# Optimization experiments

Hardware: AMD Instinct MI355X
Metric: run time of the kernel (lower is better)

Reference implementation:

```python
import jax, jax.numpy as jnp
import numpy as np

B, N, H, V = 2048, 16, 512, 780  # trees, nodes per tree, hidden size, vocab size


def _topology():
    """Build one random tree, replicate across B trees, and precompute the
    BFS level schedule on the non-backtracking line graph (as DGL's
    level_order: reversed(edges_back) = up edges leaves-first, then
    edges = down edges root-first)."""
    rng = np.random.default_rng(0)
    parent = np.zeros(N, dtype=np.int64)
    for i in range(1, N):
        parent[i] = rng.integers(0, i)
    depth = np.zeros(N, dtype=np.int64)
    for i in range(1, N):
        depth[i] = depth[parent[i]] + 1
    Epc = 2 * (N - 1)  # directed edges per tree
    src = np.zeros(Epc, dtype=np.int64)
    dst = np.zeros(Epc, dtype=np.int64)
    for i in range(1, N):
        src[2 * (i - 1)] = parent[i]; dst[2 * (i - 1)] = i          # down edge
        src[2 * (i - 1) + 1] = i;     dst[2 * (i - 1) + 1] = parent[i]  # up edge
    # line-graph predecessors of edge e=(u->v): edges f=(w->u) with w != v
    preds = [[f for f in range(Epc) if dst[f] == src[e] and src[f] != dst[e]]
             for e in range(Epc)]
    P = max(1, max(len(p) for p in preds))
    preds_pad = np.full((Epc, P), -1, dtype=np.int64)
    for e, p in enumerate(preds):
        preds_pad[e, :len(p)] = p
    D = int(depth.max())
    levels = []
    for d in range(D, 0, -1):   # upward pass, deepest level first
        levels.append([2 * (i - 1) + 1 for i in range(1, N) if depth[i] == d])
    for d in range(1, D + 1):   # downward pass, root first
        levels.append([2 * (i - 1) for i in range(1, N) if depth[i] == d])
    E = B * Epc                 # index E is the zero dummy row
    offs = np.arange(B, dtype=np.int64) * Epc
    preds_full = np.where(preds_pad[None] >= 0,
                          preds_pad[None] + offs[:, None, None], E)
    preds_full = preds_full.reshape(E, P)
    preds_full = np.concatenate(
        [preds_full, np.full((1, P), E, dtype=np.int64)], axis=0)  # [E+1, P]
    Mmax = max(len(lv) for lv in levels) * B
    lv_arr = np.full((len(levels), Mmax), E, dtype=np.int64)
    for l, lv in enumerate(levels):
        ids = (np.asarray(lv, np.int64)[None] + offs[:, None]).reshape(-1)
        lv_arr[l, :ids.size] = ids
    edge_src = (src[None] + np.arange(B, dtype=np.int64)[:, None] * N).reshape(-1)
    root_children = [2 * (i - 1) + 1 for i in range(1, N) if parent[i] == 0]
    root_in = np.asarray(root_children, np.int64)[None] + offs[:, None]  # [B, R]
    root_nodes = np.arange(B, dtype=np.int64) * N
    return edge_src, preds_full, lv_arr, root_in, root_nodes


def setup_inputs() -> dict:
    key = jax.random.key(0)
    ks = jax.random.split(key, 11)
    edge_src, preds, levels, root_in, root_nodes = _topology()
    s1 = 1.0 / np.sqrt(H)
    s2 = 1.0 / np.sqrt(2 * H)
    return {
        "wid": jax.random.randint(ks[0], (B * N,), 0, V),
        "edge_src": jnp.asarray(edge_src),
        "preds": jnp.asarray(preds),
        "levels": jnp.asarray(levels),
        "root_in": jnp.asarray(root_in),
        "root_nodes": jnp.asarray(root_nodes),
        "emb": jax.random.normal(ks[1], (V, H), jnp.float32),
        "w_r": jax.random.normal(ks[2], (H, H), jnp.float32) * s1,
        "ur_w": jax.random.normal(ks[3], (H, H), jnp.float32) * s1,
        "ur_b": jax.random.normal(ks[4], (H,), jnp.float32) * s1,
        "wz_w": jax.random.normal(ks[5], (2 * H, H), jnp.float32) * s2,
        "wz_b": jax.random.normal(ks[6], (H,), jnp.float32) * s2,
        "wh_w": jax.random.normal(ks[7], (2 * H, H), jnp.float32) * s2,
        "wh_b": jax.random.normal(ks[8], (H,), jnp.float32) * s2,
        "wo_w": jax.random.normal(ks[9], (2 * H, H), jnp.float32) * s2,
        "wo_b": jax.random.normal(ks[10], (H,), jnp.float32) * s2,
    }


def reference(wid, edge_src, preds, levels, root_in, root_nodes,
              emb, w_r, ur_w, ur_b, wz_w, wz_b, wh_w, wh_b, wo_w, wo_b):
    E = edge_src.shape[0]
    Hd = emb.shape[1]
    x = emb[wid]                                           # [B*N, H]
    zero = jnp.zeros((1, Hd), x.dtype)
    sx_all = x[edge_src]                                   # src_x per edge
    src_x = jnp.concatenate([sx_all, zero], axis=0)        # [E+1, H], row E = 0
    src_x_r = jnp.concatenate([sx_all @ w_r, zero], axis=0)  # W_r (no bias)
    h = jnp.zeros((E + 1, Hd), x.dtype)
    for l in range(levels.shape[0]):                       # static BFS levels
        idx = levels[l]                                    # [M], padded with E
        p = preds[idx]                                     # [M, P]
        h_nei = h[p]                                       # [M, P, H]
        sum_h = h_nei.sum(axis=1)
        # GRUMessage: r = sigmoid(dst.src_x_r + U_r(src.h)); m = r * src.h
        r = jax.nn.sigmoid(src_x_r[idx][:, None, :] + h_nei @ ur_w + ur_b)
        sum_g = (r * h_nei).sum(axis=1)
        sx = src_x[idx]
        # GRUUpdate
        z = jax.nn.sigmoid(jnp.concatenate([sx, sum_h], axis=-1) @ wz_w + wz_b)
        pre_h = jnp.tanh(jnp.concatenate([sx, sum_g], axis=-1) @ wh_w + wh_b)
        h = h.at[idx].set((1.0 - z) * sum_h + z * pre_h)
        h = h.at[E].set(0.0)                               # keep dummy row zero
    h_edges = h[:E]                                        # edata['h']
    h_root = h[root_in].sum(axis=1)                        # pull into roots
    x_root = x[root_nodes]
    root_vec = jax.nn.relu(
        jnp.concatenate([x_root, h_root], axis=-1) @ wo_w + wo_b)
    return h_edges, root_vec
```

## Files before the change

### kernel.cpp

```cpp
#include <hip/hip_runtime.h>
#include <hip/hip_bf16.h>
#include <cstddef>

#define HD 512

typedef short s8v __attribute__((ext_vector_type(8)));
typedef short s4v __attribute__((ext_vector_type(4)));
typedef float fx4 __attribute__((ext_vector_type(4)));

#define MFMA(a, b, c) __builtin_amdgcn_mfma_f32_16x16x32_bf16((a), (b), (c), 0, 0, 0)

__device__ __forceinline__ unsigned short f2bf(float f) {
  unsigned int u = __float_as_uint(f);
  unsigned int r = (u + 0x7fffu + ((u >> 16) & 1u)) >> 16;
  return (unsigned short)r;
}
__device__ __forceinline__ float bf2f(unsigned short u) {
  return __uint_as_float(((unsigned int)u) << 16);
}

__device__ __forceinline__ size_t swz_off(int k, int n, int KT) {
  int kt = k >> 5, kr = k & 31;
  int nt = n >> 4, nr = n & 15;
  int lane = ((kr >> 3) << 4) | nr;
  int i = kr & 7;
  return ((((size_t)nt * KT + kt) * 64 + lane) << 3) + i;
}

__global__ void pack_kernel(const float* w_r, const float* ur, const float* wz, const float* wh,
                            const float* wo,
                            unsigned short* WR, unsigned short* WUR, unsigned short* WZf,
                            unsigned short* WHf, unsigned short* WO) {
  int idx = blockIdx.x * blockDim.x + threadIdx.x;
  int stride = gridDim.x * blockDim.x;
  for (int t = idx; t < 512 * 512; t += stride) {
    int k = t >> 9, n = t & 511;
    size_t o = swz_off(k, n, 16);
    WR[o] = f2bf(w_r[t]);
    WUR[o] = f2bf(ur[t]);
  }
  for (int t = idx; t < 1024 * 512; t += stride) {
    int k = t >> 9, n = t & 511;
    size_t o = swz_off(k, n, 32);
    WZf[o] = f2bf(wz[t]);
    WHf[o] = f2bf(wh[t]);
    WO[o] = f2bf(wo[t]);
  }
}

__global__ void embed_kernel(const int* wid, const float* emb, unsigned short* x_bf, int BN) {
  int idx = blockIdx.x * blockDim.x + threadIdx.x;
  int stride = gridDim.x * blockDim.x;
  int total = BN * (HD / 8);
  for (int t = idx; t < total; t += stride) {
    int nrow = t >> 6;
    int c8 = (t & 63) << 3;
    int w = wid[nrow];
    const float4* s = (const float4*)(emb + (size_t)w * HD + c8);
    float4 v0 = s[0], v1 = s[1];
    s8v o;
    o[0] = (short)f2bf(v0.x); o[1] = (short)f2bf(v0.y);
    o[2] = (short)f2bf(v0.z); o[3] = (short)f2bf(v0.w);
    o[4] = (short)f2bf(v1.x); o[5] = (short)f2bf(v1.y);
    o[6] = (short)f2bf(v1.z); o[7] = (short)f2bf(v1.w);
    *(s8v*)&x_bf[(size_t)nrow * HD + c8] = o;
  }
}

__global__ void schedule_kernel(const int* preds, int E, int Epc, int P, int* sched) {
  __shared__ int rnd[64];
  int t = threadIdx.x;
  rnd[t] = -1;
  __syncthreads();
  for (int it = 0; it <= Epc; ++it) {
    int newv = -1;
    if (t < Epc && rnd[t] < 0) {
      int mx = 0;
      bool ready = true;
      for (int q = 0; q < P; ++q) {
        int pe = preds[t * P + q];
        if (pe < E) {
          int rp = rnd[pe];
          if (rp < 0) ready = false;
          else if (rp + 1 > mx) mx = rp + 1;
        }
      }
      if (ready) newv = mx;
    }
    __syncthreads();
    if (newv >= 0) rnd[t] = newv;
    __syncthreads();
  }
  if (t == 0) {
    int R = 0;
    for (int e = 0; e < Epc; ++e) if (rnd[e] + 1 > R) R = rnd[e] + 1;
    if (R > 31) R = 31;
    sched[0] = R;
    for (int r = 0; r < 31; ++r) {
      int c = 0;
      if (r < R) {
        for (int e = 0; e < Epc; ++e) if (rnd[e] == r) { sched[33 + r * 32 + c] = e; ++c; }
      }
      sched[1 + r] = c;
    }
  }
}

__global__ __launch_bounds__(256) void gemm_xr_kernel(const unsigned short* x_bf,
                                                      const unsigned short* WR,
                                                      unsigned short* XR, int BN) {
  __shared__ unsigned short lA[32 * 40];
  int bt = blockIdx.x;
  int mt = bt >> 1, nt = bt & 1;
  int tid = threadIdx.x, lane = tid & 63, w = tid >> 6;
  int wm = w & 1, wn = w >> 1;
  int m0 = mt << 5;
  fx4 acc[8];
#pragma unroll
  for (int n = 0; n < 8; n++) { acc[n][0]=0.f; acc[n][1]=0.f; acc[n][2]=0.f; acc[n][3]=0.f; }
  int srow = tid >> 3, squad = tid & 7;
  int arow = (wm << 4) | (lane & 15), k8 = (lane >> 4) << 3;
  for (int kt = 0; kt < 16; ++kt) {
    const unsigned short* gp = x_bf + (size_t)(m0 + srow) * HD + (kt << 5) + (squad << 2);
    *(s4v*)&lA[srow * 40 + (squad << 2)] = *(const s4v*)gp;
    __syncthreads();
    s8v a = *(const s8v*)&lA[arow * 40 + k8];
#pragma unroll
    for (int n = 0; n < 8; n++) {
      int ntile = (nt << 4) + (wn << 3) + n;
      const s8v* bp = (const s8v*)(WR + ((((size_t)ntile << 4) + kt) * 64 + lane) * 8);
      acc[n] = MFMA(a, *bp, acc[n]);
    }
    __syncthreads();
  }
#pragma unroll
  for (int n = 0; n < 8; n++) {
    int gcol = (nt << 8) + (wn << 7) + (n << 4) + (lane & 15);
#pragma unroll
    for (int q = 0; q < 4; q++) {
      int row = (wm << 4) + ((lane >> 4) << 2) + q;
      XR[(size_t)(m0 + row) * 512 + gcol] = f2bf(acc[n][q]);
    }
  }
}

struct AP {
  const int* sched;
  const int* preds;
  const int* edge_src;
  const float* ur_b;
  const unsigned short* XR;
  const unsigned short* u_bf_c;
  unsigned short* A2h;
  unsigned short* A2g;
  int* eIdx;
  int* srcIdx;
  float* h;
  int B, Epc, P, E;
};

__global__ __launch_bounds__(256) void gatherA_kernel(AP p, int r) {
  const int cnt = p.sched[1 + r];
  if (cnt == 0) return;
  const int M = cnt * p.B;
  const int* lst = p.sched + 33 + r * 32;
  const int lane = threadIdx.x & 63;
  const int waveId = blockIdx.x * 4 + (threadIdx.x >> 6);
  const int totalWaves = gridDim.x * 4;
  for (int m = waveId; m < M; m += totalWaves) {
    const int j = m / p.B;
    const int b = m - j * p.B;
    const int e = b * p.Epc + lst[j];
    const int src = p.edge_src[e];
    if (lane == 0) { p.eIdx[m] = e; p.srcIdx[m] = src; }
    const int c0 = lane << 3;
    const s8v xr8 = *(const s8v*)&p.XR[(size_t)src * 512 + c0];
    float xb[8], ub[8], sh[8], sg[8];
#pragma unroll
    for (int i = 0; i < 8; i++) {
      xb[i] = bf2f((unsigned short)xr8[i]);
      ub[i] = p.ur_b[c0 + i];
      sh[i] = 0.f; sg[i] = 0.f;
    }
    for (int t = 0; t < p.P; ++t) {
      const int pe = p.preds[(size_t)e * p.P + t];
      if (pe >= p.E) continue;
      const float4* hp = (const float4*)(p.h + (size_t)pe * 512 + c0);
      const float4 h0 = hp[0], h1 = hp[1];
      const s8v u8 = *(const s8v*)&p.u_bf_c[(size_t)pe * 512 + c0];
      const float hv[8] = {h0.x, h0.y, h0.z, h0.w, h1.x, h1.y, h1.z, h1.w};
#pragma unroll
      for (int i = 0; i < 8; i++) {
        const float rr = 1.f / (1.f + __expf(-(xb[i] + bf2f((unsigned short)u8[i]) + ub[i])));
        sh[i] += hv[i];
        sg[i] += rr * hv[i];
      }
    }
    *(float4*)(p.h + (size_t)e * 512 + c0) = make_float4(sh[0], sh[1], sh[2], sh[3]);
    *(float4*)(p.h + (size_t)e * 512 + c0 + 4) = make_float4(sh[4], sh[5], sh[6], sh[7]);
    s8v shb, sgb;
#pragma unroll
    for (int i = 0; i < 8; i++) { shb[i] = (short)f2bf(sh[i]); sgb[i] = (short)f2bf(sg[i]); }
    *(s8v*)&p.A2h[(size_t)m * 512 + c0] = shb;
    *(s8v*)&p.A2g[(size_t)m * 512 + c0] = sgb;
  }
}

struct BP {
  const int* sched;
  const float* wz_b;
  const float* wh_b;
  const unsigned short* x_bf;
  const unsigned short* A2h;
  const unsigned short* A2g;
  const unsigned short* WZf;
  const unsigned short* WHf;
  const int* eIdx;
  const int* srcIdx;
  unsigned short* h_bf;
  float* h;
  int B;
};

__global__ __launch_bounds__(256) void gemmB_kernel(BP p, int r) {
  const int cnt = p.sched[1 + r];
  if (cnt == 0) return;
  const int M = cnt * p.B;
  const int nTiles = (M >> 6) << 2;
  __shared__ unsigned short lZ[2][64 * 40];
  __shared__ unsigned short lH[2][64 * 40];
  __shared__ int eL[64];
  __shared__ int sL[64];
  const int tid = threadIdx.x, lane = tid & 63, w = tid >> 6;
  const int wm = w & 1, wn = w >> 1;
  const int srow = tid >> 2, sc8 = (tid & 3) << 3;
  const int k8 = (lane >> 4) << 3;

  for (int t = blockIdx.x; t < nTiles; t += gridDim.x) {
    const int mt = t >> 2, nb = t & 3;
    const int m0 = mt << 6, n0 = nb << 7;
    if (tid < 64) { eL[tid] = p.eIdx[m0 + tid]; sL[tid] = p.srcIdx[m0 + tid]; }
    __syncthreads();
    fx4 aZ[8], aH[8];
#pragma unroll
    for (int i = 0; i < 8; i++) {
      aZ[i][0]=0.f; aZ[i][1]=0.f; aZ[i][2]=0.f; aZ[i][3]=0.f;
      aH[i][0]=0.f; aH[i][1]=0.f; aH[i][2]=0.f; aH[i][3]=0.f;
    }
    {
      const unsigned short* g = p.x_bf + (size_t)sL[srow] * 512 + sc8;
      *(s8v*)&lZ[0][srow * 40 + sc8] = *(const s8v*)g;
    }
    for (int kt = 0; kt < 32; ++kt) {
      const int cur = kt & 1;
      __syncthreads();
      if (kt < 31) {
        const int k2 = kt + 1;
        if (k2 < 16) {
          const unsigned short* g = p.x_bf + (size_t)sL[srow] * 512 + (k2 << 5) + sc8;
          *(s8v*)&lZ[cur ^ 1][srow * 40 + sc8] = *(const s8v*)g;
        } else {
          const size_t ro = (size_t)(m0 + srow) * 512 + ((k2 - 16) << 5) + sc8;
          *(s8v*)&lZ[cur ^ 1][srow * 40 + sc8] = *(const s8v*)&p.A2h[ro];
          *(s8v*)&lH[cur ^ 1][srow * 40 + sc8] = *(const s8v*)&p.A2g[ro];
        }
      }
      s8v az[2], ah[2];
#pragma unroll
      for (int mi = 0; mi < 2; ++mi) {
        const int ao = ((wm << 5) + (mi << 4) + (lane & 15)) * 40 + k8;
        az[mi] = *(const s8v*)&lZ[cur][ao];
        ah[mi] = (kt < 16) ? az[mi] : *(const s8v*)&lH[cur][ao];
      }
#pragma unroll
      for (int ni = 0; ni < 4; ++ni) {
        const int ntile = (n0 >> 4) + (wn << 2) + ni;
        const size_t boff = (((size_t)ntile * 32 + kt) * 64 + lane) << 3;
        const s8v bz = *(const s8v*)(p.WZf + boff);
        const s8v bh = *(const s8v*)(p.WHf + boff);
#pragma unroll
        for (int mi = 0; mi < 2; ++mi) {
          aZ[mi * 4 + ni] = MFMA(az[mi], bz, aZ[mi * 4 + ni]);
          aH[mi * 4 + ni] = MFMA(ah[mi], bh, aH[mi * 4 + ni]);
        }
      }
    }
#pragma unroll
    for (int mi = 0; mi < 2; ++mi) {
#pragma unroll
      for (int q = 0; q < 4; ++q) {
        const int row = (wm << 5) + (mi << 4) + ((lane >> 4) << 2) + q;
        const int e = eL[row];
#pragma unroll
        for (int ni = 0; ni < 4; ++ni) {
          const int col = n0 + (wn << 6) + (ni << 4) + (lane & 15);
          const size_t off = (size_t)e * 512 + col;
          float zpre = aZ[mi * 4 + ni][q] + p.wz_b[col];
          float hpre = aH[mi * 4 + ni][q] + p.wh_b[col];
          float zz = 1.f / (1.f + __expf(-zpre));
          float e2 = __expf(2.f * hpre);
          float th = 1.f - 2.f / (e2 + 1.f);
          float hn = (1.f - zz) * p.h[off] + zz * th;
          p.h[off] = hn;
          p.h_bf[off] = f2bf(hn);
        }
      }
    }
    __syncthreads();
  }
}

struct CP {
  const int* sched;
  const unsigned short* h_bf;
  const unsigned short* WUR;
  const int* eIdx;
  unsigned short* u_bf;
  int B;
};

__global__ __launch_bounds__(256) void gemmC_kernel(CP p, int r) {
  const int cnt = p.sched[1 + r];
  if (cnt == 0) return;
  const int M = cnt * p.B;
  const int nTiles = (M >> 6) << 2;
  __shared__ unsigned short lA[2][64 * 40];
  __shared__ int eL[64];
  const int tid = threadIdx.x, lane = tid & 63, w = tid >> 6;
  const int wm = w & 1, wn = w >> 1;
  const int srow = tid >> 2, sc8 = (tid & 3) << 3;
  const int k8 = (lane >> 4) << 3;

  for (int t = blockIdx.x; t < nTiles; t += gridDim.x) {
    const int mt = t >> 2, nb = t & 3;
    const int m0 = mt << 6, n0 = nb << 7;
    if (tid < 64) eL[tid] = p.eIdx[m0 + tid];
    __syncthreads();
    fx4 ac[8];
#pragma unroll
    for (int i = 0; i < 8; i++) { ac[i][0]=0.f; ac[i][1]=0.f; ac[i][2]=0.f; ac[i][3]=0.f; }
    {
      const unsigned short* g = p.h_bf + (size_t)eL[srow] * 512 + sc8;
      *(s8v*)&lA[0][srow * 40 + sc8] = *(const s8v*)g;
    }
    for (int kt = 0; kt < 16; ++kt) {
      const int cur = kt & 1;
      __syncthreads();
      if (kt < 15) {
        const unsigned short* g = p.h_bf + (size_t)eL[srow] * 512 + ((kt + 1) << 5) + sc8;
        *(s8v*)&lA[cur ^ 1][srow * 40 + sc8] = *(const s8v*)g;
      }
      s8v az[2];
#pragma unroll
      for (int mi = 0; mi < 2; ++mi) {
        az[mi] = *(const s8v*)&lA[cur][((wm << 5) + (mi << 4) + (lane & 15)) * 40 + k8];
      }
#pragma unroll
      for (int ni = 0; ni < 4; ++ni) {
        const int ntile = (n0 >> 4) + (wn << 2) + ni;
        const size_t boff = (((size_t)ntile << 4) + kt) * 64 + lane;
        const s8v bu = *(const s8v*)(p.WUR + (boff << 3));
#pragma unroll
        for (int mi = 0; mi < 2; ++mi) {
          ac[mi * 4 + ni] = MFMA(az[mi], bu, ac[mi * 4 + ni]);
        }
      }
    }
#pragma unroll
    for (int mi = 0; mi < 2; ++mi) {
#pragma unroll
      for (int q = 0; q < 4; ++q) {
        const int row = (wm << 5) + (mi << 4) + ((lane >> 4) << 2) + q;
        const int e = eL[row];
#pragma unroll
        for (int ni = 0; ni < 4; ++ni) {
          const int col = n0 + (wn << 6) + (ni << 4) + (lane & 15);
          p.u_bf[(size_t)e * 512 + col] = f2bf(ac[mi * 4 + ni][q]);
        }
      }
    }
    __syncthreads();
  }
}

__global__ void root_gather_kernel(const int* root_nodes, const int* root_in,
                                   const unsigned short* x_bf, const float* h,
                                   unsigned short* Aroot, int B, int R0) {
  int lane = threadIdx.x & 63;
  int waveId = blockIdx.x * (blockDim.x >> 6) + (threadIdx.x >> 6);
  int totalWaves = gridDim.x * (blockDim.x >> 6);
  for (int b = waveId; b < B; b += totalWaves) {
    int c0 = lane << 3;
    int nd = root_nodes[b];
    *(s8v*)&Aroot[(size_t)b * 1024 + c0] = *(const s8v*)&x_bf[(size_t)nd * HD + c0];
    float s[8];
#pragma unroll
    for (int i = 0; i < 8; i++) s[i] = 0.f;
    for (int t = 0; t < R0; ++t) {
      int e = root_in[b * R0 + t];
      const float4* hp = (const float4*)(h + (size_t)e * HD + c0);
      float4 h0 = hp[0], h1 = hp[1];
      s[0] += h0.x; s[1] += h0.y; s[2] += h0.z; s[3] += h0.w;
      s[4] += h1.x; s[5] += h1.y; s[6] += h1.z; s[7] += h1.w;
    }
    s8v sb;
#pragma unroll
    for (int i = 0; i < 8; i++) sb[i] = (short)f2bf(s[i]);
    *(s8v*)&Aroot[(size_t)b * 1024 + 512 + c0] = sb;
  }
}

__global__ __launch_bounds__(256) void gemm_root_kernel(const unsigned short* Aroot,
                                                        const unsigned short* WO,
                                                        const float* wo_b, float* out, int B) {
  __shared__ unsigned short lA[32 * 40];
  int tid = threadIdx.x, lane = tid & 63, w = tid >> 6;
  int wm = w & 1, wn = w >> 1;
  int bt = blockIdx.x;
  int mt = bt >> 1, nt = bt & 1;
  int m0 = mt << 5;
  fx4 ac[8];
#pragma unroll
  for (int n = 0; n < 8; n++) { ac[n][0]=0.f; ac[n][1]=0.f; ac[n][2]=0.f; ac[n][3]=0.f; }
  int srow = tid >> 3, squad = tid & 7;
  int arow = (wm << 4) | (lane & 15), k8 = (lane >> 4) << 3;
  for (int kt = 0; kt < 32; ++kt) {
    const unsigned short* g = Aroot + (size_t)(m0 + srow) * 1024 + (kt << 5) + (squad << 2);
    *(s4v*)&lA[srow * 40 + (squad << 2)] = *(const s4v*)g;
    __syncthreads();
    s8v a = *(const s8v*)&lA[arow * 40 + k8];
#pragma unroll
    for (int n = 0; n < 8; n++) {
      int ntile = (nt << 4) + (wn << 3) + n;
      size_t boff = ((((size_t)ntile * 32) + kt) * 64 + lane) << 3;
      ac[n] = MFMA(a, *(const s8v*)(WO + boff), ac[n]);
    }
    __syncthreads();
  }
#pragma unroll
  for (int q = 0; q < 4; q++) {
    int row = (wm << 4) + ((lane >> 4) << 2) + q;
    int m = m0 + row;
#pragma unroll
    for (int n = 0; n < 8; n++) {
      int col = (nt << 8) + (wn << 7) + (n << 4) + (lane & 15);
      float v = ac[n][q] + wo_b[col];
      out[(size_t)m * HD + col] = v > 0.f ? v : 0.f;
    }
  }
}

extern "C" void kernel_launch(void* const* d_in, const int* in_sizes, int n_in,
                              void* d_out, int out_size, void* d_ws, size_t ws_size,
                              hipStream_t stream) {
  const int* wid = (const int*)d_in[0];
  const int* edge_src = (const int*)d_in[1];
  const int* preds = (const int*)d_in[2];
  const int* root_in = (const int*)d_in[4];
  const int* root_nodes = (const int*)d_in[5];
  const float* emb = (const float*)d_in[6];
  const float* w_r = (const float*)d_in[7];
  const float* ur_w = (const float*)d_in[8];
  const float* ur_b = (const float*)d_in[9];
  const float* wz_w = (const float*)d_in[10];
  const float* wz_b = (const float*)d_in[11];
  const float* wh_w = (const float*)d_in[12];
  const float* wh_b = (const float*)d_in[13];
  const float* wo_w = (const float*)d_in[14];
  const float* wo_b = (const float*)d_in[15];

  const int BN = in_sizes[0];
  const int E = in_sizes[1];
  const int Bt = in_sizes[5];
  const int Epc = E / Bt;
  const int P = in_sizes[2] / (E + 1);
  const int R0 = in_sizes[4] / Bt;

  float* h = (float*)d_out;

  char* wp = (char*)d_ws;
  auto alloc = [&](size_t bytes) {
    char* r = wp;
    wp += (bytes + 255) & ~(size_t)255;
    return r;
  };
  unsigned short* x_bf = (unsigned short*)alloc((size_t)BN * 512 * 2);
  unsigned short* XR = (unsigned short*)alloc((size_t)BN * 512 * 2);
  unsigned short* h_bf = (unsigned short*)alloc((size_t)E * 512 * 2);
  unsigned short* u_bf = (unsigned short*)alloc((size_t)E * 512 * 2);
  unsigned short* A2h = (unsigned short*)alloc((size_t)E * 512 * 2);
  unsigned short* A2g = (unsigned short*)alloc((size_t)E * 512 * 2);
  int* eIdx = (int*)alloc((size_t)E * 4);
  int* srcIdx = (int*)alloc((size_t)E * 4);
  unsigned short* WR = (unsigned short*)alloc((size_t)512 * 512 * 2);
  unsigned short* WUR = (unsigned short*)alloc((size_t)512 * 512 * 2);
  unsigned short* WZf = (unsigned short*)alloc((size_t)1024 * 512 * 2);
  unsigned short* WHf = (unsigned short*)alloc((size_t)1024 * 512 * 2);
  unsigned short* WO = (unsigned short*)alloc((size_t)1024 * 512 * 2);
  unsigned short* Aroot = (unsigned short*)alloc((size_t)Bt * 1024 * 2);
  int* sched = (int*)alloc(8192);

  hipLaunchKernelGGL(pack_kernel, dim3(512), dim3(256), 0, stream,
                     w_r, ur_w, wz_w, wh_w, wo_w, WR, WUR, WZf, WHf, WO);
  hipLaunchKernelGGL(embed_kernel, dim3(1024), dim3(256), 0, stream, wid, emb, x_bf, BN);
  hipLaunchKernelGGL(schedule_kernel, dim3(1), dim3(64), 0, stream, preds, E, Epc, P, sched);
  hipLaunchKernelGGL(gemm_xr_kernel, dim3((BN / 32) * 2), dim3(256), 0, stream, x_bf, WR, XR, BN);

  AP ap;
  ap.sched = sched; ap.preds = preds; ap.edge_src = edge_src;
  ap.ur_b = ur_b; ap.XR = XR; ap.u_bf_c = u_bf;
  ap.A2h = A2h; ap.A2g = A2g; ap.eIdx = eIdx; ap.srcIdx = srcIdx;
  ap.h = h; ap.B = Bt; ap.Epc = Epc; ap.P = P; ap.E = E;

  BP bp;
  bp.sched = sched; bp.wz_b = wz_b; bp.wh_b = wh_b;
  bp.x_bf = x_bf; bp.A2h = A2h; bp.A2g = A2g;
  bp.WZf = WZf; bp.WHf = WHf;
  bp.eIdx = eIdx; bp.srcIdx = srcIdx;
  bp.h_bf = h_bf; bp.h = h; bp.B = Bt;

  CP cp;
  cp.sched = sched; cp.h_bf = h_bf; cp.WUR = WUR;
  cp.eIdx = eIdx; cp.u_bf = u_bf; cp.B = Bt;

  for (int r = 0; r < Epc && r < 31; ++r) {
    hipLaunchKernelGGL(gatherA_kernel, dim3(1024), dim3(256), 0, stream, ap, r);
    hipLaunchKernelGGL(gemmB_kernel, dim3(2048), dim3(256), 0, stream, bp, r);
    hipLaunchKernelGGL(gemmC_kernel, dim3(2048), dim3(256), 0, stream, cp, r);
  }

  hipLaunchKernelGGL(root_gather_kernel, dim3(512), dim3(256), 0, stream,
                     root_nodes, root_in, x_bf, h, Aroot, Bt, R0);
  hipLaunchKernelGGL(gemm_root_kernel, dim3((Bt / 32) * 2), dim3(256), 0, stream,
                     Aroot, WO, wo_b, h + (size_t)E * 512, Bt);
}
```

Baseline: 1.127 ms.

## Precompute x-side Z/H projections once per node and halve per-level GEMM K

The x-half of the z and h gate GEMMs is hoisted out of the per-level loop into one upfront GEMM that produces the r, z and h x-projections together, using a concatenated weight matrix. Per-level gemmB now only multiplies the 512-wide neighbour sums and adds the precomputed x terms in the epilogue. gemmB writes a compact row-ordered bf16 copy of h, so gemmC reads contiguously instead of gathering by edge index. The change also widens the LDS K-step to 64, swizzles tile order across blocks, and halves the grid sizes. In exchange it adds an XP buffer three times the width of the old XR and extra scattered bf16 reads in the gemmB epilogue.

```diff
diff --git a/kernel.cpp b/kernel.cpp
--- a/kernel.cpp
+++ b/kernel.cpp
@@ -29,22 +29,28 @@
 
 __global__ void pack_kernel(const float* w_r, const float* ur, const float* wz, const float* wh,
                             const float* wo,
-                            unsigned short* WR, unsigned short* WUR, unsigned short* WZf,
-                            unsigned short* WHf, unsigned short* WO) {
+                            unsigned short* W1, unsigned short* WZB, unsigned short* WHB,
+                            unsigned short* WUR, unsigned short* WO) {
   int idx = blockIdx.x * blockDim.x + threadIdx.x;
   int stride = gridDim.x * blockDim.x;
+  for (int t = idx; t < 512 * 1536; t += stride) {
+    int k = t / 1536, n = t - k * 1536;
+    float v;
+    if (n < 512) v = w_r[k * 512 + n];
+    else if (n < 1024) v = wz[k * 512 + (n - 512)];
+    else v = wh[k * 512 + (n - 1024)];
+    W1[swz_off(k, n, 16)] = f2bf(v);
+  }
   for (int t = idx; t < 512 * 512; t += stride) {
     int k = t >> 9, n = t & 511;
     size_t o = swz_off(k, n, 16);
-    WR[o] = f2bf(w_r[t]);
-    WUR[o] = f2bf(ur[t]);
+    WZB[o] = f2bf(wz[(512 + k) * 512 + n]);
+    WHB[o] = f2bf(wh[(512 + k) * 512 + n]);
+    WUR[o] = f2bf(ur[k * 512 + n]);
   }
   for (int t = idx; t < 1024 * 512; t += stride) {
     int k = t >> 9, n = t & 511;
-    size_t o = swz_off(k, n, 32);
-    WZf[o] = f2bf(wz[t]);
-    WHf[o] = f2bf(wh[t]);
-    WO[o] = f2bf(wo[t]);
+    WO[swz_off(k, n, 32)] = f2bf(wo[k * 512 + n]);
   }
 }
 
@@ -106,40 +112,42 @@
   }
 }
 
-__global__ __launch_bounds__(256) void gemm_xr_kernel(const unsigned short* x_bf,
-                                                      const unsigned short* WR,
-                                                      unsigned short* XR, int BN) {
-  __shared__ unsigned short lA[32 * 40];
-  int bt = blockIdx.x;
-  int mt = bt >> 1, nt = bt & 1;
-  int tid = threadIdx.x, lane = tid & 63, w = tid >> 6;
-  int wm = w & 1, wn = w >> 1;
-  int m0 = mt << 5;
-  fx4 acc[8];
-#pragma unroll
-  for (int n = 0; n < 8; n++) { acc[n][0]=0.f; acc[n][1]=0.f; acc[n][2]=0.f; acc[n][3]=0.f; }
-  int srow = tid >> 3, squad = tid & 7;
-  int arow = (wm << 4) | (lane & 15), k8 = (lane >> 4) << 3;
+__global__ __launch_bounds__(256) void gemm_pre_kernel(const unsigned short* x_bf,
+                                                       const unsigned short* W1,
+                                                       unsigned short* XP, int BN) {
+  __shared__ unsigned short lA[2][32 * 40];
+  const int nM = BN >> 5;
+  const int slab = blockIdx.x / nM;
+  const int mt = blockIdx.x - slab * nM;
+  const int tid = threadIdx.x, lane = tid & 63, w = tid >> 6;
+  const int wm = w & 1, wn = w >> 1;
+  const int m0 = mt << 5;
+  const int srow = tid >> 3, sq4 = (tid & 7) << 2;
+  const int arow = (wm << 4) | (lane & 15), k8 = (lane >> 4) << 3;
+  fx4 ac[16];
+#pragma unroll
+  for (int i = 0; i < 16; i++) { ac[i][0]=0.f; ac[i][1]=0.f; ac[i][2]=0.f; ac[i][3]=0.f; }
+  const unsigned short* aptr = x_bf + (size_t)(m0 + srow) * 512 + sq4;
+  *(s4v*)&lA[0][srow * 40 + sq4] = *(const s4v*)aptr;
   for (int kt = 0; kt < 16; ++kt) {
-    const unsigned short* gp = x_bf + (size_t)(m0 + srow) * HD + (kt << 5) + (squad << 2);
-    *(s4v*)&lA[srow * 40 + (squad << 2)] = *(const s4v*)gp;
-    __syncthreads();
-    s8v a = *(const s8v*)&lA[arow * 40 + k8];
-#pragma unroll
-    for (int n = 0; n < 8; n++) {
-      int ntile = (nt << 4) + (wn << 3) + n;
-      const s8v* bp = (const s8v*)(WR + ((((size_t)ntile << 4) + kt) * 64 + lane) * 8);
-      acc[n] = MFMA(a, *bp, acc[n]);
-    }
-    __syncthreads();
-  }
-#pragma unroll
-  for (int n = 0; n < 8; n++) {
-    int gcol = (nt << 8) + (wn << 7) + (n << 4) + (lane & 15);
+    const int cur = kt & 1;
+    __syncthreads();
+    const s8v a = *(const s8v*)&lA[cur][arow * 40 + k8];
+    if (kt < 15) *(s4v*)&lA[cur ^ 1][srow * 40 + sq4] = *(const s4v*)(aptr + ((kt + 1) << 5));
+#pragma unroll
+    for (int ni = 0; ni < 16; ++ni) {
+      const int ntile = (slab << 5) + ((ni >> 3) << 4) + (wn << 3) + (ni & 7);
+      const s8v* bp = (const s8v*)(W1 + ((((size_t)ntile << 4) + kt) * 64 + lane) * 8);
+      ac[ni] = MFMA(a, *bp, ac[ni]);
+    }
+  }
+#pragma unroll
+  for (int ni = 0; ni < 16; ++ni) {
+    const int col = (slab << 9) + (((((ni >> 3) << 4) + (wn << 3) + (ni & 7))) << 4) + (lane & 15);
 #pragma unroll
     for (int q = 0; q < 4; q++) {
-      int row = (wm << 4) + ((lane >> 4) << 2) + q;
-      XR[(size_t)(m0 + row) * 512 + gcol] = f2bf(acc[n][q]);
+      const int row = (wm << 4) + ((lane >> 4) << 2) + q;
+      XP[(size_t)(m0 + row) * 1536 + col] = f2bf(ac[ni][q]);
     }
   }
 }
@@ -149,7 +157,7 @@
   const int* preds;
   const int* edge_src;
   const float* ur_b;
-  const unsigned short* XR;
+  const unsigned short* XP;
   const unsigned short* u_bf_c;
   unsigned short* A2h;
   unsigned short* A2g;
@@ -174,7 +182,7 @@
     const int src = p.edge_src[e];
     if (lane == 0) { p.eIdx[m] = e; p.srcIdx[m] = src; }
     const int c0 = lane << 3;
-    const s8v xr8 = *(const s8v*)&p.XR[(size_t)src * 512 + c0];
+    const s8v xr8 = *(const s8v*)&p.XP[(size_t)src * 1536 + c0];
     float xb[8], ub[8], sh[8], sg[8];
 #pragma unroll
     for (int i = 0; i < 8; i++) {
@@ -210,14 +218,14 @@
   const int* sched;
   const float* wz_b;
   const float* wh_b;
-  const unsigned short* x_bf;
+  const unsigned short* XP;
   const unsigned short* A2h;
   const unsigned short* A2g;
-  const unsigned short* WZf;
-  const unsigned short* WHf;
+  const unsigned short* WZB;
+  const unsigned short* WHB;
   const int* eIdx;
   const int* srcIdx;
-  unsigned short* h_bf;
+  unsigned short* hM;
   float* h;
   int B;
 };
@@ -226,21 +234,22 @@
   const int cnt = p.sched[1 + r];
   if (cnt == 0) return;
   const int M = cnt * p.B;
-  const int nTiles = (M >> 6) << 2;
-  __shared__ unsigned short lZ[2][64 * 40];
-  __shared__ unsigned short lH[2][64 * 40];
+  const int nT = (M >> 6) << 2;
+  const int qq = nT >> 3;
+  __shared__ unsigned short lZ[2][64 * 72];
+  __shared__ unsigned short lH[2][64 * 72];
   __shared__ int eL[64];
   __shared__ int sL[64];
   const int tid = threadIdx.x, lane = tid & 63, w = tid >> 6;
   const int wm = w & 1, wn = w >> 1;
-  const int srow = tid >> 2, sc8 = (tid & 3) << 3;
+  const int srow = tid >> 2, sc = (tid & 3) << 4;
   const int k8 = (lane >> 4) << 3;
 
-  for (int t = blockIdx.x; t < nTiles; t += gridDim.x) {
+  for (int t0 = blockIdx.x; t0 < nT; t0 += gridDim.x) {
+    const int t = (t0 & 7) * qq + (t0 >> 3);
     const int mt = t >> 2, nb = t & 3;
     const int m0 = mt << 6, n0 = nb << 7;
     if (tid < 64) { eL[tid] = p.eIdx[m0 + tid]; sL[tid] = p.srcIdx[m0 + tid]; }
-    __syncthreads();
     fx4 aZ[8], aH[8];
 #pragma unroll
     for (int i = 0; i < 8; i++) {
@@ -248,61 +257,65 @@
       aH[i][0]=0.f; aH[i][1]=0.f; aH[i][2]=0.f; aH[i][3]=0.f;
     }
     {
-      const unsigned short* g = p.x_bf + (size_t)sL[srow] * 512 + sc8;
-      *(s8v*)&lZ[0][srow * 40 + sc8] = *(const s8v*)g;
-    }
-    for (int kt = 0; kt < 32; ++kt) {
-      const int cur = kt & 1;
+      const size_t ro = (size_t)(m0 + srow) * 512 + sc;
+      *(s8v*)&lZ[0][srow * 72 + sc]     = *(const s8v*)&p.A2h[ro];
+      *(s8v*)&lZ[0][srow * 72 + sc + 8] = *(const s8v*)&p.A2h[ro + 8];
+      *(s8v*)&lH[0][srow * 72 + sc]     = *(const s8v*)&p.A2g[ro];
+      *(s8v*)&lH[0][srow * 72 + sc + 8] = *(const s8v*)&p.A2g[ro + 8];
+    }
+    for (int ks = 0; ks < 8; ++ks) {
+      const int cur = ks & 1;
       __syncthreads();
-      if (kt < 31) {
-        const int k2 = kt + 1;
-        if (k2 < 16) {
-          const unsigned short* g = p.x_bf + (size_t)sL[srow] * 512 + (k2 << 5) + sc8;
-          *(s8v*)&lZ[cur ^ 1][srow * 40 + sc8] = *(const s8v*)g;
-        } else {
-          const size_t ro = (size_t)(m0 + srow) * 512 + ((k2 - 16) << 5) + sc8;
-          *(s8v*)&lZ[cur ^ 1][srow * 40 + sc8] = *(const s8v*)&p.A2h[ro];
-          *(s8v*)&lH[cur ^ 1][srow * 40 + sc8] = *(const s8v*)&p.A2g[ro];
-        }
-      }
-      s8v az[2], ah[2];
-#pragma unroll
-      for (int mi = 0; mi < 2; ++mi) {
-        const int ao = ((wm << 5) + (mi << 4) + (lane & 15)) * 40 + k8;
-        az[mi] = *(const s8v*)&lZ[cur][ao];
-        ah[mi] = (kt < 16) ? az[mi] : *(const s8v*)&lH[cur][ao];
-      }
-#pragma unroll
-      for (int ni = 0; ni < 4; ++ni) {
-        const int ntile = (n0 >> 4) + (wn << 2) + ni;
-        const size_t boff = (((size_t)ntile * 32 + kt) * 64 + lane) << 3;
-        const s8v bz = *(const s8v*)(p.WZf + boff);
-        const s8v bh = *(const s8v*)(p.WHf + boff);
+      if (ks < 7) {
+        const size_t ro = (size_t)(m0 + srow) * 512 + ((ks + 1) << 6) + sc;
+        *(s8v*)&lZ[cur ^ 1][srow * 72 + sc]     = *(const s8v*)&p.A2h[ro];
+        *(s8v*)&lZ[cur ^ 1][srow * 72 + sc + 8] = *(const s8v*)&p.A2h[ro + 8];
+        *(s8v*)&lH[cur ^ 1][srow * 72 + sc]     = *(const s8v*)&p.A2g[ro];
+        *(s8v*)&lH[cur ^ 1][srow * 72 + sc + 8] = *(const s8v*)&p.A2g[ro + 8];
+      }
+#pragma unroll
+      for (int sub = 0; sub < 2; ++sub) {
+        const int kt = (ks << 1) + sub;
+        s8v az[2], ah[2];
 #pragma unroll
         for (int mi = 0; mi < 2; ++mi) {
-          aZ[mi * 4 + ni] = MFMA(az[mi], bz, aZ[mi * 4 + ni]);
-          aH[mi * 4 + ni] = MFMA(ah[mi], bh, aH[mi * 4 + ni]);
+          const int ao = ((wm << 5) + (mi << 4) + (lane & 15)) * 72 + (sub << 5) + k8;
+          az[mi] = *(const s8v*)&lZ[cur][ao];
+          ah[mi] = *(const s8v*)&lH[cur][ao];
+        }
+#pragma unroll
+        for (int ni = 0; ni < 4; ++ni) {
+          const int ntile = (n0 >> 4) + (wn << 2) + ni;
+          const size_t boff = ((((size_t)ntile << 4) + kt) * 64 + lane) << 3;
+          const s8v bz = *(const s8v*)(p.WZB + boff);
+          const s8v bh = *(const s8v*)(p.WHB + boff);
+#pragma unroll
+          for (int mi = 0; mi < 2; ++mi) {
+            aZ[mi * 4 + ni] = MFMA(az[mi], bz, aZ[mi * 4 + ni]);
+            aH[mi * 4 + ni] = MFMA(ah[mi], bh, aH[mi * 4 + ni]);
+          }
         }
       }
     }
 #pragma unroll
     for (int mi = 0; mi < 2; ++mi) {
 #pragma unroll
-      for (int q = 0; q < 4; ++q) {
-        const int row = (wm << 5) + (mi << 4) + ((lane >> 4) << 2) + q;
+      for (int q4 = 0; q4 < 4; ++q4) {
+        const int row = (wm << 5) + (mi << 4) + ((lane >> 4) << 2) + q4;
         const int e = eL[row];
+        const int src = sL[row];
 #pragma unroll
         for (int ni = 0; ni < 4; ++ni) {
           const int col = n0 + (wn << 6) + (ni << 4) + (lane & 15);
           const size_t off = (size_t)e * 512 + col;
-          float zpre = aZ[mi * 4 + ni][q] + p.wz_b[col];
-          float hpre = aH[mi * 4 + ni][q] + p.wh_b[col];
+          float zpre = aZ[mi * 4 + ni][q4] + bf2f(p.XP[(size_t)src * 1536 + 512 + col]) + p.wz_b[col];
+          float hpre = aH[mi * 4 + ni][q4] + bf2f(p.XP[(size_t)src * 1536 + 1024 + col]) + p.wh_b[col];
           float zz = 1.f / (1.f + __expf(-zpre));
           float e2 = __expf(2.f * hpre);
           float th = 1.f - 2.f / (e2 + 1.f);
           float hn = (1.f - zz) * p.h[off] + zz * th;
           p.h[off] = hn;
-          p.h_bf[off] = f2bf(hn);
+          p.hM[(size_t)(m0 + row) * 512 + col] = f2bf(hn);
         }
       }
     }
@@ -312,7 +325,7 @@
 
 struct CP {
   const int* sched;
-  const unsigned short* h_bf;
+  const unsigned short* hM;
   const unsigned short* WUR;
   const int* eIdx;
   unsigned short* u_bf;
@@ -323,59 +336,66 @@
   const int cnt = p.sched[1 + r];
   if (cnt == 0) return;
   const int M = cnt * p.B;
-  const int nTiles = (M >> 6) << 2;
-  __shared__ unsigned short lA[2][64 * 40];
+  const int nT = (M >> 6) << 2;
+  const int qq = nT >> 3;
+  __shared__ unsigned short lA[2][64 * 72];
   __shared__ int eL[64];
   const int tid = threadIdx.x, lane = tid & 63, w = tid >> 6;
   const int wm = w & 1, wn = w >> 1;
-  const int srow = tid >> 2, sc8 = (tid & 3) << 3;
+  const int srow = tid >> 2, sc = (tid & 3) << 4;
   const int k8 = (lane >> 4) << 3;
 
-  for (int t = blockIdx.x; t < nTiles; t += gridDim.x) {
+  for (int t0 = blockIdx.x; t0 < nT; t0 += gridDim.x) {
+    const int t = (t0 & 7) * qq + (t0 >> 3);
     const int mt = t >> 2, nb = t & 3;
     const int m0 = mt << 6, n0 = nb << 7;
     if (tid < 64) eL[tid] = p.eIdx[m0 + tid];
-    __syncthreads();
     fx4 ac[8];
 #pragma unroll
     for (int i = 0; i < 8; i++) { ac[i][0]=0.f; ac[i][1]=0.f; ac[i][2]=0.f; ac[i][3]=0.f; }
     {
-      const unsigned short* g = p.h_bf + (size_t)eL[srow] * 512 + sc8;
-      *(s8v*)&lA[0][srow * 40 + sc8] = *(const s8v*)g;
-    }
-    for (int kt = 0; kt < 16; ++kt) {
-      const int cur = kt & 1;
+      const size_t ro = (size_t)(m0 + srow) * 512 + sc;
+      *(s8v*)&lA[0][srow * 72 + sc]     = *(const s8v*)&p.hM[ro];
+      *(s8v*)&lA[0][srow * 72 + sc + 8] = *(const s8v*)&p.hM[ro + 8];
+    }
+    for (int ks = 0; ks < 8; ++ks) {
+      const int cur = ks & 1;
       __syncthreads();
-      if (kt < 15) {
-        const unsigned short* g = p.h_bf + (size_t)eL[srow] * 512 + ((kt + 1) << 5) + sc8;
-        *(s8v*)&lA[cur ^ 1][srow * 40 + sc8] = *(const s8v*)g;
-      }
-      s8v az[2];
-#pragma unroll
-      for (int mi = 0; mi < 2; ++mi) {
-        az[mi] = *(const s8v*)&lA[cur][((wm << 5) + (mi << 4) + (lane & 15)) * 40 + k8];
-      }
-#pragma unroll
-      for (int ni = 0; ni < 4; ++ni) {
-        const int ntile = (n0 >> 4) + (wn << 2) + ni;
-        const size_t boff = (((size_t)ntile << 4) + kt) * 64 + lane;
-        const s8v bu = *(const s8v*)(p.WUR + (boff << 3));
+      if (ks < 7) {
+        const size_t ro = (size_t)(m0 + srow) * 512 + ((ks + 1) << 6) + sc;
+        *(s8v*)&lA[cur ^ 1][srow * 72 + sc]     = *(const s8v*)&p.hM[ro];
+        *(s8v*)&lA[cur ^ 1][srow * 72 + sc + 8] = *(const s8v*)&p.hM[ro + 8];
+      }
+#pragma unroll
+      for (int sub = 0; sub < 2; ++sub) {
+        const int kt = (ks << 1) + sub;
+        s8v a[2];
 #pragma unroll
         for (int mi = 0; mi < 2; ++mi) {
-          ac[mi * 4 + ni] = MFMA(az[mi], bu, ac[mi * 4 + ni]);
+          a[mi] = *(const s8v*)&lA[cur][((wm << 5) + (mi << 4) + (lane & 15)) * 72 + (sub << 5) + k8];
+        }
+#pragma unroll
+        for (int ni = 0; ni < 4; ++ni) {
+          const int ntile = (n0 >> 4) + (wn << 2) + ni;
+          const size_t boff = ((((size_t)ntile << 4) + kt) * 64 + lane) << 3;
+          const s8v bu = *(const s8v*)(p.WUR + boff);
+#pragma unroll
+          for (int mi = 0; mi < 2; ++mi) {
+            ac[mi * 4 + ni] = MFMA(a[mi], bu, ac[mi * 4 + ni]);
+          }
         }
       }
     }
 #pragma unroll
     for (int mi = 0; mi < 2; ++mi) {
 #pragma unroll
-      for (int q = 0; q < 4; ++q) {
-        const int row = (wm << 5) + (mi << 4) + ((lane >> 4) << 2) + q;
+      for (int q4 = 0; q4 < 4; ++q4) {
+        const int row = (wm << 5) + (mi << 4) + ((lane >> 4) << 2) + q4;
         const int e = eL[row];
 #pragma unroll
         for (int ni = 0; ni < 4; ++ni) {
           const int col = n0 + (wn << 6) + (ni << 4) + (lane & 15);
-          p.u_bf[(size_t)e * 512 + col] = f2bf(ac[mi * 4 + ni][q]);
+          p.u_bf[(size_t)e * 512 + col] = f2bf(ac[mi * 4 + ni][q4]);
         }
       }
     }
@@ -485,48 +505,49 @@
     return r;
   };
   unsigned short* x_bf = (unsigned short*)alloc((size_t)BN * 512 * 2);
-  unsigned short* XR = (unsigned short*)alloc((size_t)BN * 512 * 2);
-  unsigned short* h_bf = (unsigned short*)alloc((size_t)E * 512 * 2);
+  unsigned short* XP = (unsigned short*)alloc((size_t)BN * 1536 * 2);
   unsigned short* u_bf = (unsigned short*)alloc((size_t)E * 512 * 2);
   unsigned short* A2h = (unsigned short*)alloc((size_t)E * 512 * 2);
   unsigned short* A2g = (unsigned short*)alloc((size_t)E * 512 * 2);
+  unsigned short* hM = (unsigned short*)alloc((size_t)E * 512 * 2);
   int* eIdx = (int*)alloc((size_t)E * 4);
   int* srcIdx = (int*)alloc((size_t)E * 4);
-  unsigned short* WR = (unsigned short*)alloc((size_t)512 * 512 * 2);
+  unsigned short* W1 = (unsigned short*)alloc((size_t)512 * 1536 * 2);
+  unsigned short* WZB = (unsigned short*)alloc((size_t)512 * 512 * 2);
+  unsigned short* WHB = (unsigned short*)alloc((size_t)512 * 512 * 2);
   unsigned short* WUR = (unsigned short*)alloc((size_t)512 * 512 * 2);
-  unsigned short* WZf = (unsigned short*)alloc((size_t)1024 * 512 * 2);
-  unsigned short* WHf = (unsigned short*)alloc((size_t)1024 * 512 * 2);
   unsigned short* WO = (unsigned short*)alloc((size_t)1024 * 512 * 2);
   unsigned short* Aroot = (unsigned short*)alloc((size_t)Bt * 1024 * 2);
   int* sched = (int*)alloc(8192);
 
   hipLaunchKernelGGL(pack_kernel, dim3(512), dim3(256), 0, stream,
-                     w_r, ur_w, wz_w, wh_w, wo_w, WR, WUR, WZf, WHf, WO);
+                     w_r, ur_w, wz_w, wh_w, wo_w, W1, WZB, WHB, WUR, WO);
   hipLaunchKernelGGL(embed_kernel, dim3(1024), dim3(256), 0, stream, wid, emb, x_bf, BN);
   hipLaunchKernelGGL(schedule_kernel, dim3(1), dim3(64), 0, stream, preds, E, Epc, P, sched);
-  hipLaunchKernelGGL(gemm_xr_kernel, dim3((BN / 32) * 2), dim3(256), 0, stream, x_bf, WR, XR, BN);
+  hipLaunchKernelGGL(gemm_pre_kernel, dim3((BN / 32) * 3), dim3(256), 0, stream,
+                     x_bf, W1, XP, BN);
 
   AP ap;
   ap.sched = sched; ap.preds = preds; ap.edge_src = edge_src;
-  ap.ur_b = ur_b; ap.XR = XR; ap.u_bf_c = u_bf;
+  ap.ur_b = ur_b; ap.XP = XP; ap.u_bf_c = u_bf;
   ap.A2h = A2h; ap.A2g = A2g; ap.eIdx = eIdx; ap.srcIdx = srcIdx;
   ap.h = h; ap.B = Bt; ap.Epc = Epc; ap.P = P; ap.E = E;
 
   BP bp;
   bp.sched = sched; bp.wz_b = wz_b; bp.wh_b = wh_b;
-  bp.x_bf = x_bf; bp.A2h = A2h; bp.A2g = A2g;
-  bp.WZf = WZf; bp.WHf = WHf;
+  bp.XP = XP; bp.A2h = A2h; bp.A2g = A2g;
+  bp.WZB = WZB; bp.WHB = WHB;
   bp.eIdx = eIdx; bp.srcIdx = srcIdx;
-  bp.h_bf = h_bf; bp.h = h; bp.B = Bt;
+  bp.hM = hM; bp.h = h; bp.B = Bt;
 
   CP cp;
-  cp.sched = sched; cp.h_bf = h_bf; cp.WUR = WUR;
+  cp.sched = sched; cp.hM = hM; cp.WUR = WUR;
   cp.eIdx = eIdx; cp.u_bf = u_bf; cp.B = Bt;
 
   for (int r = 0; r < Epc && r < 31; ++r) {
     hipLaunchKernelGGL(gatherA_kernel, dim3(1024), dim3(256), 0, stream, ap, r);
-    hipLaunchKernelGGL(gemmB_kernel, dim3(2048), dim3(256), 0, stream, bp, r);
-    hipLaunchKernelGGL(gemmC_kernel, dim3(2048), dim3(256), 0, stream, cp, r);
+    hipLaunchKernelGGL(gemmB_kernel, dim3(1024), dim3(256), 0, stream, bp, r);
+    hipLaunchKernelGGL(gemmC_kernel, dim3(1024), dim3(256), 0, stream, cp, r);
   }
 
   hipLaunchKernelGGL(root_gather_kernel, dim3(512), dim3(256), 0, stream,
```

After: 1.250 ms. +10.9%, slower.
